# Kernel tuning notes

Hardware: AMD Instinct MI355X
Metric: run time of the kernel (lower is better)

The kernel has to match this reference:

```python
import jax, jax.numpy as jnp
import numpy as np

N_RES = 4096
BATCH = 1024
N_IN = 128
N_OUT = 64
TEACHER_SHIFT = 0.0
TEACHER_SCALE = 1.0
PREV_STATE_WEIGHT = 0.1
SPECTRAL_RADIUS = 0.95


def setup_inputs() -> dict:
    key = jax.random.key(0)
    ks = jax.random.split(key, 9)
    # Reservoir weights, scaled to fixed spectral radius (as in build()).
    W_res = jax.random.uniform(ks[0], (N_RES, N_RES), minval=-0.5, maxval=0.5, dtype=jnp.float32)
    e = jnp.linalg.eigvalsh(W_res)  # tf.linalg.eigh also treats matrix as symmetric
    W_res = W_res * (SPECTRAL_RADIUS / jnp.max(jnp.abs(e)))
    W_in = jax.random.uniform(ks[1], (N_RES, N_IN), minval=-1.0, maxval=1.0, dtype=jnp.float32)
    W_out = jax.random.uniform(ks[2], (N_RES, N_OUT), minval=-1.0, maxval=1.0, dtype=jnp.float32)
    B_in = 0.1 * jax.random.normal(ks[3], (N_RES, 1), dtype=jnp.float32)
    return {
        "passed": jax.random.normal(ks[4], (BATCH, N_IN), dtype=jnp.float32),
        "lastOutput": jax.random.normal(ks[5], (N_OUT, BATCH), dtype=jnp.float32),
        "lastPredOutput": jax.random.normal(ks[6], (N_OUT, BATCH), dtype=jnp.float32),
        "x": jax.random.normal(ks[7], (BATCH, N_RES), dtype=jnp.float32),
        "prob": 50.0 * jnp.ones((1,), dtype=jnp.float32),
        "rand_num": jax.random.uniform(ks[8], (1,), minval=1.0, maxval=100.0, dtype=jnp.float32),
        "W_in": W_in,
        "W_res": W_res,
        "W_out": W_out,
        "B_in": B_in,
    }


def reference(passed, lastOutput, lastPredOutput, x, prob, rand_num, W_in, W_res, W_out, B_in):
    # Teacher forcing selection (tf.case on random draw vs prob), applied after scale/shift.
    last_true = lastOutput * TEACHER_SCALE + TEACHER_SHIFT      # [n_out, B]
    last_pred = lastPredOutput * TEACHER_SCALE + TEACHER_SHIFT  # [n_out, B]
    toUse = jnp.where(rand_num[0] < prob[0], last_true, last_pred)  # [n_out, B]

    # Batched version of the per-sample loop:
    #   tanh(W_in@u_i + W_res@x_i + W_out@toUse[:,i] + B_in)
    pre = (passed @ W_in.T            # [B, N] input drive
           + x @ W_res.T              # [B, N] recurrent drive
           + toUse.T @ W_out.T        # [B, N] output feedback
           + B_in[:, 0][None, :])     # [1, N] bias
    new_state = PREV_STATE_WEIGHT * x + (1.0 - PREV_STATE_WEIGHT) * jnp.tanh(pre)
    return new_state  # [B, N]; original returns this split into B [1,N] tensors
```

## Files before the change

kernel.cpp:

```cpp
#include <hip/hip_runtime.h>
#include <hip/hip_bf16.h>
#include <math.h>

#define NRES   4096
#define NBATCH 1024
#define NIN    128
#define NOUT   64
#define KT     4672
#define KQ     (KT / 4)
#define TILES  73
#define MN     ((size_t)NBATCH * NRES)

typedef __bf16 bf16x8 __attribute__((ext_vector_type(8)));
typedef __bf16 bf16x4 __attribute__((ext_vector_type(4)));
typedef float  f32x4  __attribute__((ext_vector_type(4)));

__device__ __forceinline__ float lo_part(float f) {
    return f - (float)(__bf16)f;
}

__device__ __forceinline__ void gload_lds16(const __bf16* g, __bf16* l) {
    __builtin_amdgcn_global_load_lds(
        (const __attribute__((address_space(1))) unsigned int*)g,
        (__attribute__((address_space(3))) unsigned int*)l, 16, 0, 0);
}

__global__ __launch_bounds__(256) void pack_A4(
    const float* __restrict__ x, const float* __restrict__ passed,
    const float* __restrict__ lastOut, const float* __restrict__ lastPred,
    const float* __restrict__ prob, const float* __restrict__ rand_num,
    __bf16* __restrict__ Abuf)
{
    unsigned id = blockIdx.x * 256u + threadIdx.x;
    if (id >= (unsigned)NBATCH * KQ) return;
    unsigned b = id / KQ;
    unsigned k = (id - b * KQ) * 4u;
    f32x4 v;
    if (k < 4096u) {
        v = *(const f32x4*)(x + (size_t)b * NRES + k);
    } else if (k < 4224u) {
        v = *(const f32x4*)(passed + b * NIN + (k - 4096u));
    } else if (k < 4352u) {
        v = *(const f32x4*)(passed + b * NIN + (k - 4224u));
    } else if (k < 4480u) {
        f32x4 f = *(const f32x4*)(passed + b * NIN + (k - 4352u));
#pragma unroll
        for (int e = 0; e < 4; ++e) v[e] = lo_part(f[e]);
    } else {
        const float* src = (rand_num[0] < prob[0]) ? lastOut : lastPred;
#pragma unroll
        for (int e = 0; e < 4; ++e) {
            unsigned kk = k + e;
            unsigned j; bool want_lo;
            if (kk < 4544u)      { j = kk - 4480u; want_lo = false; }
            else if (kk < 4608u) { j = kk - 4544u; want_lo = false; }
            else                 { j = kk - 4608u; want_lo = true;  }
            float f = src[j * NBATCH + b];
            v[e] = want_lo ? lo_part(f) : f;
        }
    }
    bf16x4 o;
#pragma unroll
    for (int e = 0; e < 4; ++e) o[e] = (__bf16)v[e];
    *(bf16x4*)(Abuf + (size_t)id * 4u) = o;
}

__global__ __launch_bounds__(256) void pack_B4(
    const float* __restrict__ W_res, const float* __restrict__ W_in,
    const float* __restrict__ W_out, __bf16* __restrict__ Bbuf)
{
    unsigned id = blockIdx.x * 256u + threadIdx.x;
    if (id >= (unsigned)NRES * KQ) return;
    unsigned n = id / KQ;
    unsigned k = (id - n * KQ) * 4u;
    f32x4 v;
    if (k < 4096u) {
        v = *(const f32x4*)(W_res + (size_t)n * NRES + k);
    } else if (k < 4224u) {
        v = *(const f32x4*)(W_in + n * NIN + (k - 4096u));
    } else if (k < 4352u) {
        f32x4 f = *(const f32x4*)(W_in + n * NIN + (k - 4224u));
#pragma unroll
        for (int e = 0; e < 4; ++e) v[e] = lo_part(f[e]);
    } else if (k < 4480u) {
        v = *(const f32x4*)(W_in + n * NIN + (k - 4352u));
    } else if (k < 4544u) {
        v = *(const f32x4*)(W_out + n * NOUT + (k - 4480u));
    } else if (k < 4608u) {
        f32x4 f = *(const f32x4*)(W_out + n * NOUT + (k - 4544u));
#pragma unroll
        for (int e = 0; e < 4; ++e) v[e] = lo_part(f[e]);
    } else {
        v = *(const f32x4*)(W_out + n * NOUT + (k - 4608u));
    }
    bf16x4 o;
#pragma unroll
    for (int e = 0; e < 4; ++e) o[e] = (__bf16)v[e];
    *(bf16x4*)(Bbuf + (size_t)id * 4u) = o;
}

__global__ __launch_bounds__(512, 1) void gemm_kernel(
    const __bf16* __restrict__ Abuf, const __bf16* __restrict__ Bbuf,
    float* __restrict__ part, int split)
{
    __shared__ __align__(16) __bf16 SH[2][32768];

    const int t  = threadIdx.x;
    const int l  = t & 63;
    const int w  = t >> 6;
    const int wm = w >> 2;
    const int wn = w & 3;
    const int bn = blockIdx.x, bm = blockIdx.y, bz = blockIdx.z;
    const int qs = TILES / split, rs = TILES % split;
    const int t0 = bz * qs + (bz < rs ? bz : rs);
    const int nt = qs + (bz < rs ? 1 : 0);

    f32x4 acc[8][4] = {};

    unsigned gA[4], gB[4];
    int lA[4], lB[4];
#pragma unroll
    for (int j = 0; j < 4; ++j) {
        int ca  = j * 512 + t;
        int row = ca >> 3;
        int cb  = (ca & 7) << 4;
        int cs  = cb ^ ((row & 7) << 4);
        gA[j] = (unsigned)((bm * 256 + row) * KT) + (cs >> 1);
        gB[j] = (unsigned)((bn * 256 + row) * KT) + (cs >> 1);
        lA[j] = ca * 8;
        lB[j] = 16384 + ca * 8;
    }

#define STAGE_ALL(nxt, k0n)                                              \
    do {                                                                 \
        _Pragma("unroll")                                                \
        for (int j = 0; j < 4; ++j)                                      \
            gload_lds16(Abuf + gA[j] + (k0n), &SH[nxt][lA[j]]);          \
        _Pragma("unroll")                                                \
        for (int j = 0; j < 4; ++j)                                      \
            gload_lds16(Bbuf + gB[j] + (k0n), &SH[nxt][lB[j]]);          \
    } while (0)

    int eA[8], eB[4];
#pragma unroll
    for (int m = 0; m < 8; ++m) {
        int row = wm * 128 + m * 16 + (l & 15);
        eA[m] = row * 64 + (((((l >> 4) << 4)) ^ ((row & 7) << 4)) >> 1);
    }
#pragma unroll
    for (int n = 0; n < 4; ++n) {
        int col = wn * 64 + n * 16 + (l & 15);
        eB[n] = 16384 + col * 64 + (((((l >> 4) << 4)) ^ ((col & 7) << 4)) >> 1);
    }

    bf16x8 af[4][2], bfr[4][2];

#define BAR() do { asm volatile("" ::: "memory");                        \
                   __builtin_amdgcn_s_barrier();                         \
                   asm volatile("" ::: "memory"); } while (0)

#define LDA(qd, buf)                                                     \
    do {                                                                 \
        _Pragma("unroll")                                                \
        for (int m2 = 0; m2 < 4; ++m2) {                                 \
            af[m2][0] = *(const bf16x8*)&SH[buf][eA[(qd)*4 + m2]];       \
            af[m2][1] = *(const bf16x8*)&SH[buf][eA[(qd)*4 + m2] ^ 32];  \
        }                                                                \
    } while (0)

#define LDB(h, buf)                                                      \
    do {                                                                 \
        _Pragma("unroll")                                                \
        for (int n3 = 0; n3 < 2; ++n3) {                                 \
            bfr[(h)*2+n3][0] = *(const bf16x8*)&SH[buf][eB[(h)*2 + n3]]; \
            bfr[(h)*2+n3][1] = *(const bf16x8*)&SH[buf][eB[(h)*2+n3] ^ 32]; \
        }                                                                \
    } while (0)

#define MFMA16(qm, qn)                                                   \
    do {                                                                 \
        __builtin_amdgcn_s_setprio(1);                                   \
        _Pragma("unroll")                                                \
        for (int kk2 = 0; kk2 < 2; ++kk2)                                \
            _Pragma("unroll")                                            \
            for (int m2 = 0; m2 < 4; ++m2)                               \
                _Pragma("unroll")                                        \
                for (int n2 = 0; n2 < 2; ++n2)                           \
                    acc[(qm)*4+m2][(qn)*2+n2] =                          \
                        __builtin_amdgcn_mfma_f32_16x16x32_bf16(         \
                            af[m2][kk2], bfr[(qn)*2+n2][kk2],            \
                            acc[(qm)*4+m2][(qn)*2+n2], 0, 0, 0);         \
        __builtin_amdgcn_s_setprio(0);                                   \
    } while (0)

    STAGE_ALL(0, t0 * 64);
    asm volatile("s_waitcnt vmcnt(0)" ::: "memory");
    BAR();

    for (int tt = 0; tt < nt; ++tt) {
        const int cur = tt & 1;
        const int nxt = cur ^ 1;
        const bool pf = (tt + 1 < nt);
        if (pf) STAGE_ALL(nxt, (t0 + tt + 1) * 64);
        LDA(0, cur); LDB(0, cur);
        BAR();
        MFMA16(0, 0);
        BAR();
        LDB(1, cur);
        BAR();
        MFMA16(0, 1);
        BAR();
        LDA(1, cur);
        BAR();
        MFMA16(1, 0);
        BAR();
        if (pf) asm volatile("s_waitcnt vmcnt(0)" ::: "memory");
        BAR();
        MFMA16(1, 1);
    }

    float* pz = part + (size_t)bz * MN;
    const int r0 = bm * 256 + wm * 128 + ((l >> 4) << 2);
    const int c0 = bn * 256 + wn * 64 + (l & 15);
#pragma unroll
    for (int m = 0; m < 8; ++m) {
#pragma unroll
        for (int i = 0; i < 4; ++i) {
            float* prow = pz + (size_t)(r0 + m * 16 + i) * NRES;
#pragma unroll
            for (int n = 0; n < 4; ++n)
                prow[c0 + n * 16] = acc[m][n][i];
        }
    }
#undef STAGE_ALL
#undef BAR
#undef LDA
#undef LDB
#undef MFMA16
}

__global__ __launch_bounds__(256) void epilogue_kernel(
    const float* __restrict__ part, int split, const float* __restrict__ xin,
    const float* __restrict__ Bin, float* __restrict__ out)
{
    size_t id = (size_t)blockIdx.x * 256u + threadIdx.x;
    size_t e  = id * 4;
    int c = (int)(e & (NRES - 1));
    f32x4 s = *(const f32x4*)(part + e);
    for (int z = 1; z < split; ++z) {
        f32x4 p = *(const f32x4*)(part + (size_t)z * MN + e);
        s += p;
    }
    f32x4 xv = *(const f32x4*)(xin + e);
    f32x4 bv = *(const f32x4*)(Bin + c);
    f32x4 o;
#pragma unroll
    for (int j = 0; j < 4; ++j)
        o[j] = 0.1f * xv[j] + 0.9f * tanhf(s[j] + bv[j]);
    *(f32x4*)(out + e) = o;
}

extern "C" void kernel_launch(void* const* d_in, const int* in_sizes, int n_in,
                              void* d_out, int out_size, void* d_ws, size_t ws_size,
                              hipStream_t stream) {
    (void)in_sizes; (void)n_in; (void)out_size;
    const float* passed     = (const float*)d_in[0];
    const float* lastOutput = (const float*)d_in[1];
    const float* lastPred   = (const float*)d_in[2];
    const float* x          = (const float*)d_in[3];
    const float* prob       = (const float*)d_in[4];
    const float* rand_num   = (const float*)d_in[5];
    const float* W_in       = (const float*)d_in[6];
    const float* W_res      = (const float*)d_in[7];
    const float* W_out      = (const float*)d_in[8];
    const float* B_in       = (const float*)d_in[9];
    float* out = (float*)d_out;

    const size_t AB = (size_t)(NBATCH + NRES) * KT * 2;
    __bf16* Abuf = (__bf16*)d_ws;
    __bf16* Bbuf = (__bf16*)((char*)d_ws + (size_t)NBATCH * KT * 2);
    float*  part = (float*)((char*)d_ws + AB);

    int split = 1;
    if (ws_size >= AB + 4 * MN * sizeof(float))      split = 4;
    else if (ws_size >= AB + 2 * MN * sizeof(float)) split = 2;

    pack_A4<<<(NBATCH * KQ) / 256, 256, 0, stream>>>(
        x, passed, lastOutput, lastPred, prob, rand_num, Abuf);
    pack_B4<<<(NRES * KQ) / 256, 256, 0, stream>>>(
        W_res, W_in, W_out, Bbuf);

    dim3 grid(NRES / 256, NBATCH / 256, split);
    gemm_kernel<<<grid, 512, 0, stream>>>(Abuf, Bbuf, part, split);

    epilogue_kernel<<<4096, 256, 0, stream>>>(part, split, x, B_in, out);
}
```

Baseline: 86.07 us.

## Interleave per-quarter global-to-LDS prefetch with MFMA phases using partial vmcnt waits

Splits each tile's global-to-LDS staging into four quarter chunks, two A row groups and two B column groups, each issued next to the MFMA phase that consumes it. Waits use partial vmcnt counts instead of one full drain per tile, and the last tile is peeled out of the loop. The goal is to spread memory traffic across the compute phases and hide load latency. In exchange the wait counting and barrier placement become more fragile, and a wrong count could read LDS data that has not landed yet.

```diff
diff --git a/kernel.cpp b/kernel.cpp
--- a/kernel.cpp
+++ b/kernel.cpp
@@ -117,28 +117,37 @@
 
     f32x4 acc[8][4] = {};
 
-    unsigned gA[4], gB[4];
-    int lA[4], lB[4];
-#pragma unroll
-    for (int j = 0; j < 4; ++j) {
-        int ca  = j * 512 + t;
-        int row = ca >> 3;
-        int cb  = (ca & 7) << 4;
-        int cs  = cb ^ ((row & 7) << 4);
-        gA[j] = (unsigned)((bm * 256 + row) * KT) + (cs >> 1);
-        gB[j] = (unsigned)((bn * 256 + row) * KT) + (cs >> 1);
-        lA[j] = ca * 8;
-        lB[j] = 16384 + ca * 8;
-    }
-
-#define STAGE_ALL(nxt, k0n)                                              \
+    unsigned goff[4][2];
+    int lE[4][2];
+#pragma unroll
+    for (int c = 0; c < 4; ++c) {
+#pragma unroll
+        for (int j = 0; j < 2; ++j) {
+            int ui = j * 512 + t;
+            int lr = ui >> 3;
+            int cb = (ui & 7) << 4;
+            int rc;
+            if (c == 0)      rc = (lr & 63) + ((lr >> 6) << 7);
+            else if (c == 1) rc = 64 + (lr & 63) + ((lr >> 6) << 7);
+            else if (c == 2) rc = (lr & 31) + ((lr >> 5) << 6);
+            else             rc = 32 + (lr & 31) + ((lr >> 5) << 6);
+            int cs = cb ^ ((rc & 7) << 4);
+            if (c < 2) {
+                goff[c][j] = (unsigned)((bm * 256 + rc) * KT) + (cs >> 1);
+                lE[c][j]   = rc * 64 + (cb >> 1);
+            } else {
+                goff[c][j] = (unsigned)((bn * 256 + rc) * KT) + (cs >> 1);
+                lE[c][j]   = 16384 + rc * 64 + (cb >> 1);
+            }
+        }
+    }
+
+#define STAGEC(c, nxt, k0n)                                              \
     do {                                                                 \
-        _Pragma("unroll")                                                \
-        for (int j = 0; j < 4; ++j)                                      \
-            gload_lds16(Abuf + gA[j] + (k0n), &SH[nxt][lA[j]]);          \
-        _Pragma("unroll")                                                \
-        for (int j = 0; j < 4; ++j)                                      \
-            gload_lds16(Bbuf + gB[j] + (k0n), &SH[nxt][lB[j]]);          \
+        gload_lds16(((c) < 2 ? Abuf : Bbuf) + goff[c][0] + (k0n),        \
+                    &SH[nxt][lE[c][0]]);                                 \
+        gload_lds16(((c) < 2 ? Abuf : Bbuf) + goff[c][1] + (k0n),        \
+                    &SH[nxt][lE[c][1]]);                                 \
     } while (0)
 
     int eA[8], eB[4];
@@ -158,6 +167,7 @@
 #define BAR() do { asm volatile("" ::: "memory");                        \
                    __builtin_amdgcn_s_barrier();                         \
                    asm volatile("" ::: "memory"); } while (0)
+#define VM(n) asm volatile("s_waitcnt vmcnt(" #n ")" ::: "memory")
 
 #define LDA(qd, buf)                                                     \
     do {                                                                 \
@@ -193,28 +203,55 @@
         __builtin_amdgcn_s_setprio(0);                                   \
     } while (0)
 
-    STAGE_ALL(0, t0 * 64);
-    asm volatile("s_waitcnt vmcnt(0)" ::: "memory");
-    BAR();
-
-    for (int tt = 0; tt < nt; ++tt) {
+    {
+        const int k00 = t0 * 64;
+        STAGEC(0, 0, k00); STAGEC(2, 0, k00); STAGEC(3, 0, k00); STAGEC(1, 0, k00);
+        VM(4);
+        BAR();
+    }
+
+    for (int tt = 0; tt < nt - 1; ++tt) {
         const int cur = tt & 1;
         const int nxt = cur ^ 1;
-        const bool pf = (tt + 1 < nt);
-        if (pf) STAGE_ALL(nxt, (t0 + tt + 1) * 64);
+        const int k0n = (t0 + tt + 1) * 64;
         LDA(0, cur); LDB(0, cur);
+        STAGEC(0, nxt, k0n);
+        VM(4);
         BAR();
         MFMA16(0, 0);
         BAR();
         LDB(1, cur);
+        STAGEC(2, nxt, k0n);
+        VM(4);
         BAR();
         MFMA16(0, 1);
         BAR();
         LDA(1, cur);
+        STAGEC(3, nxt, k0n);
         BAR();
         MFMA16(1, 0);
         BAR();
-        if (pf) asm volatile("s_waitcnt vmcnt(0)" ::: "memory");
+        STAGEC(1, nxt, k0n);
+        VM(4);
+        BAR();
+        MFMA16(1, 1);
+        BAR();
+    }
+    {
+        const int cur = (nt - 1) & 1;
+        LDA(0, cur); LDB(0, cur);
+        VM(2);
+        BAR();
+        MFMA16(0, 0);
+        BAR();
+        LDB(1, cur);
+        VM(0);
+        BAR();
+        MFMA16(0, 1);
+        BAR();
+        LDA(1, cur);
+        BAR();
+        MFMA16(1, 0);
         BAR();
         MFMA16(1, 1);
     }
@@ -232,8 +269,9 @@
                 prow[c0 + n * 16] = acc[m][n][i];
         }
     }
-#undef STAGE_ALL
+#undef STAGEC
 #undef BAR
+#undef VM
 #undef LDA
 #undef LDB
 #undef MFMA16
```

New measurement: 84.07 us. 1.02x faster.
